# Optimization experiments

Measured on AMD Instinct MI355X. Metric: run time of the kernel, lower is better.

## Reference

```python
import jax, jax.numpy as jnp
import numpy as np

N = 100000      # nodes
E = 3200000     # edges (avg degree 32)
F = 256         # input features
C = 256         # output channels


def setup_inputs() -> dict:
    key = jax.random.key(0)
    k1, k2, k3, k4, k5 = jax.random.split(key, 5)
    x = jax.random.normal(k1, (N, F), dtype=jnp.float32)
    edge_row = jax.random.randint(k2, (E,), 0, N, dtype=jnp.int32)
    edge_col = jax.random.randint(k3, (E,), 0, N, dtype=jnp.int32)
    # precomputed normalized adjacency values (D^-1/2 (A+I) D^-1/2 entries)
    edge_vals = jax.random.uniform(k4, (E,), dtype=jnp.float32)
    kernel = jax.random.normal(k5, (F, C), dtype=jnp.float32) * (1.0 / np.sqrt(F))
    bias = jnp.zeros((C,), dtype=jnp.float32)
    return {"x": x, "edge_row": edge_row, "edge_col": edge_col,
            "edge_vals": edge_vals, "kernel": kernel, "bias": bias}


def reference(x, edge_row, edge_col, edge_vals, kernel, bias):
    # GraphConv: Z = relu( A_hat @ (X @ W) + b ), single mode, sparse A_hat.
    h = x @ kernel                                   # [N, C]
    msgs = edge_vals[:, None] * h[edge_col]          # [E, C] gather along cols
    agg = jax.ops.segment_sum(msgs, edge_row, num_segments=N)  # [N, C]
    return jax.nn.relu(agg + bias)
```

## Files before the change

### kernel.cpp

```cpp
#include <hip/hip_runtime.h>
#include <hip/hip_bf16.h>
#include <hip/hip_fp16.h>


#define CAP 2432
#define NBMAX 1600
#define CH_A3 8192
#define D1_SMEM 19200

typedef __attribute__((ext_vector_type(4))) float f32x4;
typedef __attribute__((ext_vector_type(8))) short s16x8;

__device__ __forceinline__ unsigned short f2bf(float f) {
    unsigned u = __float_as_uint(f);
    u += 0x7FFFu + ((u >> 16) & 1u);
    return (unsigned short)(u >> 16);
}
__device__ __forceinline__ float bf2f(unsigned short s) {
    return __uint_as_float(((unsigned)s) << 16);
}

__global__ __launch_bounds__(256) void k_pre(const float* __restrict__ W,
                                             unsigned short* __restrict__ Wt,
                                             int* __restrict__ gcur, int NB) {
    int bid = blockIdx.x, t = threadIdx.x;
    if (bid < 256) {
        int idx = bid * 256 + t;
        int k = idx >> 8, c = idx & 255;
        Wt[c * 256 + k] = f2bf(W[idx]);
    } else {
        for (int j = t; j < NB; j += 256) gcur[j] = 0;
    }
}

__device__ __forceinline__ void a3_body(const int* __restrict__ row,
                                        const int* __restrict__ col,
                                        const float* __restrict__ val,
                                        int* __restrict__ gcur,
                                        unsigned* __restrict__ bcv,
                                        unsigned char* __restrict__ blr,
                                        int E, int NB, int chunk, char* smem) {
    int* h    = (int*)smem;
    int* base = h + NBMAX;
    int* cur  = base + NBMAX;
    int t = threadIdx.x;
    for (int j = t; j < NB; j += 256) { h[j] = 0; cur[j] = 0; }
    __syncthreads();
    int start = chunk * CH_A3;
    int end = min(E, start + CH_A3);
    for (int i = start + t; i < end; i += 256)
        atomicAdd(&h[row[i] >> 6], 1);
    __syncthreads();
    for (int j = t; j < NB; j += 256) {
        int c = h[j];
        base[j] = c ? atomicAdd(&gcur[j], c) : 0;
    }
    __syncthreads();
    for (int i = start + t; i < end; i += 256) {
        int r = row[i];
        int b = r >> 6;
        int ofs = atomicAdd(&cur[b], 1);
        size_t idx = (size_t)b * CAP + base[b] + ofs;
        unsigned hb = (unsigned)__half_as_ushort(__float2half(val[i]));
        bcv[idx] = (unsigned)col[i] | (hb << 17);
        blr[idx] = (unsigned char)(r & 63);
    }
}

__device__ __forceinline__ void gemm_body(const float* __restrict__ X,
                                          const unsigned short* __restrict__ Wt,
                                          unsigned short* __restrict__ H,
                                          int M, int g, char* smem) {
    typedef unsigned short AsRow[40];
    AsRow* As = (AsRow*)smem;
    int t = threadIdx.x;
    int lane = t & 63;
    int w = t >> 6;
    int r0 = g * 64;
    int c0 = w * 64;
    int srow = t >> 2;
    int sslot = t & 3;
    int gr = r0 + srow; if (gr >= M) gr = M - 1;

    f32x4 acc[4][4] = {};

    for (int k0 = 0; k0 < 256; k0 += 32) {
        const float* p = &X[(size_t)gr * 256 + k0 + sslot * 8];
        f32x4 a0 = __builtin_nontemporal_load((const f32x4*)p);
        f32x4 a1 = __builtin_nontemporal_load((const f32x4*)(p + 4));
        s16x8 va;
        va[0] = (short)f2bf(a0[0]); va[1] = (short)f2bf(a0[1]);
        va[2] = (short)f2bf(a0[2]); va[3] = (short)f2bf(a0[3]);
        va[4] = (short)f2bf(a1[0]); va[5] = (short)f2bf(a1[1]);
        va[6] = (short)f2bf(a1[2]); va[7] = (short)f2bf(a1[3]);
        __syncthreads();
        *(s16x8*)&As[srow][sslot * 8] = va;
        __syncthreads();

        int kofs = (lane >> 4) * 8;
        s16x8 afr[4], bfr[4];
#pragma unroll
        for (int mi = 0; mi < 4; ++mi)
            afr[mi] = *(const s16x8*)&As[mi * 16 + (lane & 15)][kofs];
#pragma unroll
        for (int ni = 0; ni < 4; ++ni) {
            int cn = c0 + ni * 16 + (lane & 15);
            bfr[ni] = *(const s16x8*)&Wt[(size_t)cn * 256 + k0 + kofs];
        }
#pragma unroll
        for (int mi = 0; mi < 4; ++mi)
#pragma unroll
            for (int ni = 0; ni < 4; ++ni)
                acc[mi][ni] = __builtin_amdgcn_mfma_f32_16x16x32_bf16(
                    afr[mi], bfr[ni], acc[mi][ni], 0, 0, 0);
    }

#pragma unroll
    for (int mi = 0; mi < 4; ++mi) {
#pragma unroll
        for (int ni = 0; ni < 4; ++ni) {
            int rg = r0 + mi * 16 + (lane >> 4) * 4;
            int cg = c0 + ni * 16 + (lane & 15);
#pragma unroll
            for (int j = 0; j < 4; ++j) {
                if (rg + j < M)
                    H[(size_t)(rg + j) * 256 + cg] = f2bf(acc[mi][ni][j]);
            }
        }
    }
}

__global__ __launch_bounds__(256) void kD1(const int* __restrict__ row,
                                           const int* __restrict__ col,
                                           const float* __restrict__ val,
                                           int* __restrict__ gcur,
                                           unsigned* __restrict__ bcv,
                                           unsigned char* __restrict__ blr,
                                           int E, int NB, int nA3,
                                           const float* __restrict__ X,
                                           const unsigned short* __restrict__ Wt,
                                           unsigned short* __restrict__ H, int M) {
    extern __shared__ char smem[];
    int bid = blockIdx.x;
    if (bid < nA3) {
        a3_body(row, col, val, gcur, bcv, blr, E, NB, bid, smem);
        return;
    }
    gemm_body(X, Wt, H, M, bid - nA3, smem);
}

__global__ __launch_bounds__(256) void kD2(const unsigned* __restrict__ bcv,
                                           const unsigned char* __restrict__ blr,
                                           const int* __restrict__ gcur,
                                           const unsigned short* __restrict__ H,
                                           const float* __restrict__ bias,
                                           float* __restrict__ out, int N) {
    __shared__ int cnt[64], rs[64], cur[64];
    __shared__ unsigned csr[CAP];
    int b = blockIdx.x;
    int t = threadIdx.x;
    size_t gb = (size_t)b * CAP;
    int n = gcur[b];

    if (t < 64) cnt[t] = 0;
    __syncthreads();
    for (int i = t; i < n; i += 256)
        atomicAdd(&cnt[blr[gb + i]], 1);
    __syncthreads();
    if (t < 64) rs[t] = cnt[t];
    __syncthreads();
    for (int off = 1; off < 64; off <<= 1) {
        int tmp = (t < 64 && t >= off) ? rs[t - off] : 0;
        __syncthreads();
        if (t < 64 && t >= off) rs[t] += tmp;
        __syncthreads();
    }
    if (t < 64) {
        int ex = rs[t] - cnt[t];
        rs[t] = ex;
        cur[t] = ex;
    }
    __syncthreads();
    for (int i = t; i < n; i += 256) {
        unsigned cv = bcv[gb + i];
        int lr = blr[gb + i];
        int ofs = atomicAdd(&cur[lr], 1);
        csr[ofs] = cv;
    }
    __syncthreads();

    int wave = t >> 6;
    int lane = t & 63;
    int h = lane >> 5;
    int cbase = (lane & 31) * 8;

#define ACC(K, HV)                                                      \
    {                                                                   \
        float v = __half2float(__ushort_as_half((unsigned short)((K) >> 17))); \
        a0 += v * bf2f((unsigned short)(HV)[0]);                        \
        a1 += v * bf2f((unsigned short)(HV)[1]);                        \
        a2 += v * bf2f((unsigned short)(HV)[2]);                        \
        a3 += v * bf2f((unsigned short)(HV)[3]);                        \
        a4 += v * bf2f((unsigned short)(HV)[4]);                        \
        a5 += v * bf2f((unsigned short)(HV)[5]);                        \
        a6 += v * bf2f((unsigned short)(HV)[6]);                        \
        a7 += v * bf2f((unsigned short)(HV)[7]);                        \
    }

    for (int rr = 0; rr < 16; ++rr) {
        int r = wave * 16 + rr;
        int node = b * 64 + r;
        if (node >= N) break;
        int s = rs[r];
        int e = s + cnt[r];

        float a0=0.f,a1=0.f,a2=0.f,a3=0.f,a4=0.f,a5=0.f,a6=0.f,a7=0.f;

        int i = s;
        for (; i + 7 < e; i += 8) {
            unsigned k0 = csr[i + h];
            unsigned k1 = csr[i + 2 + h];
            unsigned k2 = csr[i + 4 + h];
            unsigned k3 = csr[i + 6 + h];
            s16x8 g0 = *(const s16x8*)&H[(k0 & 0x1FFFFu) * 256 + cbase];
            s16x8 g1 = *(const s16x8*)&H[(k1 & 0x1FFFFu) * 256 + cbase];
            s16x8 g2 = *(const s16x8*)&H[(k2 & 0x1FFFFu) * 256 + cbase];
            s16x8 g3 = *(const s16x8*)&H[(k3 & 0x1FFFFu) * 256 + cbase];
            ACC(k0, g0); ACC(k1, g1); ACC(k2, g2); ACC(k3, g3);
        }
        for (; i + 1 < e; i += 2) {
            unsigned k0 = csr[i + h];
            s16x8 g0 = *(const s16x8*)&H[(k0 & 0x1FFFFu) * 256 + cbase];
            ACC(k0, g0);
        }
        if (i < e) {
            unsigned k0 = csr[i];
            s16x8 g0 = *(const s16x8*)&H[(k0 & 0x1FFFFu) * 256 + cbase];
            float v = h ? 0.f
                        : __half2float(__ushort_as_half((unsigned short)(k0 >> 17)));
            a0 += v * bf2f((unsigned short)g0[0]);
            a1 += v * bf2f((unsigned short)g0[1]);
            a2 += v * bf2f((unsigned short)g0[2]);
            a3 += v * bf2f((unsigned short)g0[3]);
            a4 += v * bf2f((unsigned short)g0[4]);
            a5 += v * bf2f((unsigned short)g0[5]);
            a6 += v * bf2f((unsigned short)g0[6]);
            a7 += v * bf2f((unsigned short)g0[7]);
        }

        a0 += __shfl_xor(a0, 32); a1 += __shfl_xor(a1, 32);
        a2 += __shfl_xor(a2, 32); a3 += __shfl_xor(a3, 32);
        a4 += __shfl_xor(a4, 32); a5 += __shfl_xor(a5, 32);
        a6 += __shfl_xor(a6, 32); a7 += __shfl_xor(a7, 32);

        float w0 = h ? a4 : a0;
        float w1 = h ? a5 : a1;
        float w2 = h ? a6 : a2;
        float w3 = h ? a7 : a3;
        int cw = cbase + h * 4;
        float4 b4 = *(const float4*)&bias[cw];
        float4 o;
        o.x = fmaxf(w0 + b4.x, 0.f);
        o.y = fmaxf(w1 + b4.y, 0.f);
        o.z = fmaxf(w2 + b4.z, 0.f);
        o.w = fmaxf(w3 + b4.w, 0.f);
        *(float4*)&out[(size_t)node * 256 + cw] = o;
    }
#undef ACC
}

extern "C" void kernel_launch(void* const* d_in, const int* in_sizes, int n_in,
                              void* d_out, int out_size, void* d_ws, size_t ws_size,
                              hipStream_t stream) {
    const float* x     = (const float*)d_in[0];
    const int*   erow  = (const int*)d_in[1];
    const int*   ecol  = (const int*)d_in[2];
    const float* evals = (const float*)d_in[3];
    const float* W     = (const float*)d_in[4];
    const float* bias  = (const float*)d_in[5];
    float* out = (float*)d_out;

    const int C = 256;
    const int N = in_sizes[0] / C;
    const int E = in_sizes[1];
    const int NB = (N + 63) / 64;

    char* ws = (char*)d_ws;
    size_t off = 0;
    auto carve = [&](size_t bytes) -> void* {
        void* p = ws + off;
        off += (bytes + 255) & ~(size_t)255;
        return p;
    };
    unsigned short* Hbf = (unsigned short*)carve((size_t)N * C * 2);
    unsigned short* Wt  = (unsigned short*)carve((size_t)C * 256 * 2);
    int*            gcur= (int*)carve((size_t)NB * 4);
    unsigned*       bcv = (unsigned*)carve((size_t)NB * CAP * 4);
    unsigned char*  blr = (unsigned char*)carve((size_t)NB * CAP);

    int nA3 = (E + CH_A3 - 1) / CH_A3;
    int gemmBlocks = (N + 63) / 64;

    k_pre<<<257, 256, 0, stream>>>(W, Wt, gcur, NB);
    kD1<<<nA3 + gemmBlocks, 256, D1_SMEM, stream>>>(erow, ecol, evals, gcur,
                                                    bcv, blr, E, NB, nA3,
                                                    x, Wt, Hbf, N);
    kD2<<<NB, 256, 0, stream>>>(bcv, blr, gcur, Hbf, bias, out, N);
}
```

Baseline: 386.7 us.

## Split bucket sort and aggregation into separate kernels with one node per wave

The fused sort-and-aggregate kernel becomes two kernels. The first sorts each 64-node bucket in place in global memory, using per-wave histograms to reduce LDS atomic contention, and writes per-node row offsets and counts. The second kernel gives each wave one node, so blocks are small and many, which should balance load and raise occupancy compared with one block serially processing 64 nodes. The cost is an extra launch plus a global write and re-read of the sorted edge array.

```diff
diff --git a/kernel.cpp b/kernel.cpp
--- a/kernel.cpp
+++ b/kernel.cpp
@@ -149,50 +149,77 @@
     gemm_body(X, Wt, H, M, bid - nA3, smem);
 }
 
-__global__ __launch_bounds__(256) void kD2(const unsigned* __restrict__ bcv,
+__global__ __launch_bounds__(256) void kB2(unsigned* __restrict__ bcv,
                                            const unsigned char* __restrict__ blr,
                                            const int* __restrict__ gcur,
-                                           const unsigned short* __restrict__ H,
-                                           const float* __restrict__ bias,
-                                           float* __restrict__ out, int N) {
-    __shared__ int cnt[64], rs[64], cur[64];
-    __shared__ unsigned csr[CAP];
+                                           int2* __restrict__ rowinfo, int N) {
+    __shared__ unsigned scv[CAP];
+    __shared__ unsigned char slr[CAP];
+    __shared__ int hist[4][64];
+    __shared__ int rs[64], cnt[64];
     int b = blockIdx.x;
     int t = threadIdx.x;
+    int w = t >> 6;
     size_t gb = (size_t)b * CAP;
     int n = gcur[b];
 
-    if (t < 64) cnt[t] = 0;
-    __syncthreads();
-    for (int i = t; i < n; i += 256)
-        atomicAdd(&cnt[blr[gb + i]], 1);
-    __syncthreads();
-    if (t < 64) rs[t] = cnt[t];
-    __syncthreads();
-    for (int off = 1; off < 64; off <<= 1) {
-        int tmp = (t < 64 && t >= off) ? rs[t - off] : 0;
-        __syncthreads();
-        if (t < 64 && t >= off) rs[t] += tmp;
-        __syncthreads();
-    }
-    if (t < 64) {
-        int ex = rs[t] - cnt[t];
-        rs[t] = ex;
-        cur[t] = ex;
-    }
+    if (t < 64) { hist[0][t] = 0; hist[1][t] = 0; hist[2][t] = 0; hist[3][t] = 0; }
     __syncthreads();
     for (int i = t; i < n; i += 256) {
         unsigned cv = bcv[gb + i];
-        int lr = blr[gb + i];
-        int ofs = atomicAdd(&cur[lr], 1);
-        csr[ofs] = cv;
-    }
-    __syncthreads();
-
-    int wave = t >> 6;
-    int lane = t & 63;
+        unsigned char lr = blr[gb + i];
+        scv[i] = cv;
+        slr[i] = lr;
+        atomicAdd(&hist[w][lr], 1);
+    }
+    __syncthreads();
+    if (t < 64) {
+        int h0 = hist[0][t], h1 = hist[1][t], h2 = hist[2][t], h3 = hist[3][t];
+        cnt[t] = h0 + h1 + h2 + h3;
+        rs[t] = cnt[t];
+        hist[0][t] = 0;
+        hist[1][t] = h0;
+        hist[2][t] = h0 + h1;
+        hist[3][t] = h0 + h1 + h2;
+    }
+    __syncthreads();
+    for (int off = 1; off < 64; off <<= 1) {
+        int v = (t < 64 && t >= off) ? rs[t - off] : 0;
+        __syncthreads();
+        if (t < 64 && t >= off) rs[t] += v;
+        __syncthreads();
+    }
+    if (t < 64) {
+        int st = rs[t] - cnt[t];
+        hist[0][t] += st; hist[1][t] += st;
+        hist[2][t] += st; hist[3][t] += st;
+        int node = b * 64 + t;
+        if (node < N) rowinfo[node] = make_int2((int)(gb + st), cnt[t]);
+    }
+    __syncthreads();
+    for (int i = t; i < n; i += 256) {
+        int lr = slr[i];
+        int pos = atomicAdd(&hist[w][lr], 1);
+        bcv[gb + pos] = scv[i];
+    }
+}
+
+__global__ __launch_bounds__(256) void k_agg(const unsigned short* __restrict__ H,
+                                             const int2* __restrict__ rowinfo,
+                                             const unsigned* __restrict__ csr,
+                                             const float* __restrict__ bias,
+                                             float* __restrict__ out, int n) {
+    int wave = threadIdx.x >> 6;
+    int lane = threadIdx.x & 63;
+    int node = blockIdx.x * 4 + wave;
+    if (node >= n) return;
+    int2 ri = rowinfo[node];
+    int s = ri.x;
+    int e = ri.x + ri.y;
     int h = lane >> 5;
     int cbase = (lane & 31) * 8;
+
+    float a0=0.f,a1=0.f,a2=0.f,a3=0.f,a4=0.f,a5=0.f,a6=0.f,a7=0.f;
 
 #define ACC(K, HV)                                                      \
     {                                                                   \
@@ -207,66 +234,56 @@
         a7 += v * bf2f((unsigned short)(HV)[7]);                        \
     }
 
-    for (int rr = 0; rr < 16; ++rr) {
-        int r = wave * 16 + rr;
-        int node = b * 64 + r;
-        if (node >= N) break;
-        int s = rs[r];
-        int e = s + cnt[r];
-
-        float a0=0.f,a1=0.f,a2=0.f,a3=0.f,a4=0.f,a5=0.f,a6=0.f,a7=0.f;
-
-        int i = s;
-        for (; i + 7 < e; i += 8) {
-            unsigned k0 = csr[i + h];
-            unsigned k1 = csr[i + 2 + h];
-            unsigned k2 = csr[i + 4 + h];
-            unsigned k3 = csr[i + 6 + h];
-            s16x8 g0 = *(const s16x8*)&H[(k0 & 0x1FFFFu) * 256 + cbase];
-            s16x8 g1 = *(const s16x8*)&H[(k1 & 0x1FFFFu) * 256 + cbase];
-            s16x8 g2 = *(const s16x8*)&H[(k2 & 0x1FFFFu) * 256 + cbase];
-            s16x8 g3 = *(const s16x8*)&H[(k3 & 0x1FFFFu) * 256 + cbase];
-            ACC(k0, g0); ACC(k1, g1); ACC(k2, g2); ACC(k3, g3);
-        }
-        for (; i + 1 < e; i += 2) {
-            unsigned k0 = csr[i + h];
-            s16x8 g0 = *(const s16x8*)&H[(k0 & 0x1FFFFu) * 256 + cbase];
-            ACC(k0, g0);
-        }
-        if (i < e) {
-            unsigned k0 = csr[i];
-            s16x8 g0 = *(const s16x8*)&H[(k0 & 0x1FFFFu) * 256 + cbase];
-            float v = h ? 0.f
-                        : __half2float(__ushort_as_half((unsigned short)(k0 >> 17)));
-            a0 += v * bf2f((unsigned short)g0[0]);
-            a1 += v * bf2f((unsigned short)g0[1]);
-            a2 += v * bf2f((unsigned short)g0[2]);
-            a3 += v * bf2f((unsigned short)g0[3]);
-            a4 += v * bf2f((unsigned short)g0[4]);
-            a5 += v * bf2f((unsigned short)g0[5]);
-            a6 += v * bf2f((unsigned short)g0[6]);
-            a7 += v * bf2f((unsigned short)g0[7]);
-        }
-
-        a0 += __shfl_xor(a0, 32); a1 += __shfl_xor(a1, 32);
-        a2 += __shfl_xor(a2, 32); a3 += __shfl_xor(a3, 32);
-        a4 += __shfl_xor(a4, 32); a5 += __shfl_xor(a5, 32);
-        a6 += __shfl_xor(a6, 32); a7 += __shfl_xor(a7, 32);
-
-        float w0 = h ? a4 : a0;
-        float w1 = h ? a5 : a1;
-        float w2 = h ? a6 : a2;
-        float w3 = h ? a7 : a3;
-        int cw = cbase + h * 4;
-        float4 b4 = *(const float4*)&bias[cw];
-        float4 o;
-        o.x = fmaxf(w0 + b4.x, 0.f);
-        o.y = fmaxf(w1 + b4.y, 0.f);
-        o.z = fmaxf(w2 + b4.z, 0.f);
-        o.w = fmaxf(w3 + b4.w, 0.f);
-        *(float4*)&out[(size_t)node * 256 + cw] = o;
+    int i = s;
+    for (; i + 7 < e; i += 8) {
+        unsigned k0 = csr[i + h];
+        unsigned k1 = csr[i + 2 + h];
+        unsigned k2 = csr[i + 4 + h];
+        unsigned k3 = csr[i + 6 + h];
+        s16x8 g0 = *(const s16x8*)&H[(k0 & 0x1FFFFu) * 256 + cbase];
+        s16x8 g1 = *(const s16x8*)&H[(k1 & 0x1FFFFu) * 256 + cbase];
+        s16x8 g2 = *(const s16x8*)&H[(k2 & 0x1FFFFu) * 256 + cbase];
+        s16x8 g3 = *(const s16x8*)&H[(k3 & 0x1FFFFu) * 256 + cbase];
+        ACC(k0, g0); ACC(k1, g1); ACC(k2, g2); ACC(k3, g3);
+    }
+    for (; i + 1 < e; i += 2) {
+        unsigned k0 = csr[i + h];
+        s16x8 g0 = *(const s16x8*)&H[(k0 & 0x1FFFFu) * 256 + cbase];
+        ACC(k0, g0);
+    }
+    if (i < e) {
+        unsigned k0 = csr[i];
+        s16x8 g0 = *(const s16x8*)&H[(k0 & 0x1FFFFu) * 256 + cbase];
+        float v = h ? 0.f
+                    : __half2float(__ushort_as_half((unsigned short)(k0 >> 17)));
+        a0 += v * bf2f((unsigned short)g0[0]);
+        a1 += v * bf2f((unsigned short)g0[1]);
+        a2 += v * bf2f((unsigned short)g0[2]);
+        a3 += v * bf2f((unsigned short)g0[3]);
+        a4 += v * bf2f((unsigned short)g0[4]);
+        a5 += v * bf2f((unsigned short)g0[5]);
+        a6 += v * bf2f((unsigned short)g0[6]);
+        a7 += v * bf2f((unsigned short)g0[7]);
     }
 #undef ACC
+
+    a0 += __shfl_xor(a0, 32); a1 += __shfl_xor(a1, 32);
+    a2 += __shfl_xor(a2, 32); a3 += __shfl_xor(a3, 32);
+    a4 += __shfl_xor(a4, 32); a5 += __shfl_xor(a5, 32);
+    a6 += __shfl_xor(a6, 32); a7 += __shfl_xor(a7, 32);
+
+    float w0 = h ? a4 : a0;
+    float w1 = h ? a5 : a1;
+    float w2 = h ? a6 : a2;
+    float w3 = h ? a7 : a3;
+    int cw = cbase + h * 4;
+    float4 b4 = *(const float4*)&bias[cw];
+    float4 o;
+    o.x = fmaxf(w0 + b4.x, 0.f);
+    o.y = fmaxf(w1 + b4.y, 0.f);
+    o.z = fmaxf(w2 + b4.z, 0.f);
+    o.w = fmaxf(w3 + b4.w, 0.f);
+    *(float4*)&out[(size_t)node * 256 + cw] = o;
 }
 
 extern "C" void kernel_launch(void* const* d_in, const int* in_sizes, int n_in,
@@ -297,6 +314,7 @@
     int*            gcur= (int*)carve((size_t)NB * 4);
     unsigned*       bcv = (unsigned*)carve((size_t)NB * CAP * 4);
     unsigned char*  blr = (unsigned char*)carve((size_t)NB * CAP);
+    int2*           rinf= (int2*)carve((size_t)N * 8);
 
     int nA3 = (E + CH_A3 - 1) / CH_A3;
     int gemmBlocks = (N + 63) / 64;
@@ -305,5 +323,6 @@
     kD1<<<nA3 + gemmBlocks, 256, D1_SMEM, stream>>>(erow, ecol, evals, gcur,
                                                     bcv, blr, E, NB, nA3,
                                                     x, Wt, Hbf, N);
-    kD2<<<NB, 256, 0, stream>>>(bcv, blr, gcur, Hbf, bias, out, N);
-}
+    kB2<<<NB, 256, 0, stream>>>(bcv, blr, gcur, rinf, N);
+    k_agg<<<(N + 3) / 4, 256, 0, stream>>>(Hbf, rinf, bcv, bias, out, N);
+}
```

After: 378.9 us. -2.0%, faster.
